# Kernel optimization log

Hardware: AMD Instinct MI355X
Metric: run time of the kernel (lower is better)

The kernel has to match this reference:

```python
import jax, jax.numpy as jnp
import numpy as np

EPS = 1e-8  # matches PairwiseCosine eps clamp


def setup_inputs() -> dict:
    key = jax.random.key(0)
    k1, k2, k3 = jax.random.split(key, 3)
    B, N, M, D = 8, 2048, 2048, 256
    desc_src = jax.random.normal(k1, (B, N, D), dtype=jnp.float32)
    desc_dst = jax.random.normal(k2, (B, M, D), dtype=jnp.float32)
    points_dst = jax.random.uniform(k3, (B, M, 2), dtype=jnp.float32)
    return {"desc_src": desc_src, "desc_dst": desc_dst, "points_dst": points_dst}


def reference(desc_src, desc_dst, points_dst):
    # Pairwise cosine similarity: [B, N, M]
    xx = jnp.linalg.norm(desc_src, axis=-1, keepdims=True)          # [B, N, 1]
    yy = jnp.linalg.norm(desc_dst, axis=-1, keepdims=True)          # [B, M, 1]
    xy = jnp.einsum('bnd,bmd->bnm', desc_src, desc_dst)             # [B, N, M]
    sim = xy / jnp.maximum(xx * jnp.swapaxes(yy, 1, 2), EPS)
    # Best match per source descriptor
    confidence = jnp.max(sim, axis=2)                               # [B, N]
    idx = jnp.argmax(sim, axis=2)                                   # [B, N]
    # Gather matched destination points: [B, N, 2]
    matched = jnp.take_along_axis(points_dst, idx[:, :, None], axis=1)
    return (matched, confidence)
```

## Files before the change

### kernel.cpp

```cpp
#include <hip/hip_runtime.h>
#include <stdint.h>

constexpr int Bq = 8, Nq = 2048, Mq = 2048, Dq = 256;
constexpr int TILE = 128;
constexpr int KC = 32;
constexpr int NCH = Dq / KC;
constexpr size_t ROWS = (size_t)Bq * Nq;
constexpr size_t ARR = ROWS * Dq;

typedef float f32x4 __attribute__((ext_vector_type(4)));
typedef _Float16 f16x8 __attribute__((ext_vector_type(8)));
typedef __fp16 fp16x2 __attribute__((ext_vector_type(2)));

typedef const __attribute__((address_space(1))) void* as1_t;
typedef __attribute__((address_space(3))) void* as3_t;

__device__ __forceinline__ void gl_lds16(const void* g, void* l) {
  __builtin_amdgcn_global_load_lds((as1_t)g, (as3_t)l, 16, 0, 0);
}

__device__ __forceinline__ uint32_t f2sortable(float f) {
  uint32_t u = __float_as_uint(f);
  return (u & 0x80000000u) ? ~u : (u | 0x80000000u);
}
__device__ __forceinline__ float sortable2f(uint32_t s) {
  uint32_t u = (s & 0x80000000u) ? (s ^ 0x80000000u) : ~s;
  return __uint_as_float(u);
}

__global__ __launch_bounds__(256)
void split_kernel(const float* __restrict__ src, const float* __restrict__ dst,
                  uint16_t* __restrict__ Ahg, uint16_t* __restrict__ Alg,
                  uint16_t* __restrict__ Bhg, uint16_t* __restrict__ Blg,
                  float* __restrict__ inv_ns, float* __restrict__ inv_nd) {
  int w = blockIdx.x * 4 + (threadIdx.x >> 6);
  int lane = threadIdx.x & 63;
  bool isB = w >= (int)ROWS;
  int row = isB ? (w - (int)ROWS) : w;
  const float* p = (isB ? dst : src) + (size_t)row * Dq + lane * 4;
  float4 v = *(const float4*)p;
  float x[4] = {v.x, v.y, v.z, v.w};
  float sq = 0.f;
  union { fp16x2 p2[2]; uint2 u; } H, L;
#pragma unroll
  for (int j = 0; j < 2; ++j) {
    float x0 = x[2 * j], x1 = x[2 * j + 1];
    sq = fmaf(x0, x0, sq);
    sq = fmaf(x1, x1, sq);
    float h0 = __uint_as_float(__float_as_uint(x0) & 0xFFFFE000u);
    float h1 = __uint_as_float(__float_as_uint(x1) & 0xFFFFE000u);
    H.p2[j] = __builtin_amdgcn_cvt_pkrtz(h0, h1);
    L.p2[j] = __builtin_amdgcn_cvt_pkrtz(x0 - h0, x1 - h1);
  }
  uint16_t* hp = (isB ? Bhg : Ahg) + (size_t)row * Dq + lane * 4;
  uint16_t* lp = (isB ? Blg : Alg) + (size_t)row * Dq + lane * 4;
  *(uint2*)hp = H.u;
  *(uint2*)lp = L.u;
#pragma unroll
  for (int m = 32; m >= 1; m >>= 1) sq += __shfl_xor(sq, m);
  if (lane == 0) {
    float inv = 1.0f / sqrtf(sq);
    (isB ? inv_nd : inv_ns)[row] = inv;
  }
}

__global__ __launch_bounds__(256, 4)
void simmax_kernel(const uint16_t* __restrict__ Ahg, const uint16_t* __restrict__ Alg,
                   const uint16_t* __restrict__ Bhg, const uint16_t* __restrict__ Blg,
                   const float* __restrict__ inv_ns, const float* __restrict__ inv_nd,
                   unsigned long long* __restrict__ best) {
  __shared__ __align__(16) _Float16 lds[4][TILE][KC];

  const int b = blockIdx.z, nt = blockIdx.y, mt = blockIdx.x;
  const int tid = threadIdx.x;
  const int lane = tid & 63;
  const int wave = tid >> 6;
  const int wy = wave >> 1, wx = wave & 1;
  const int ln15 = lane & 15, lq = lane >> 4;

  const uint16_t* garr = (wave == 0) ? Ahg : (wave == 1) ? Alg
                        : (wave == 2) ? Bhg : Blg;
  const int rowg0 = (wave < 2) ? (b * Nq + nt * TILE) : (b * Mq + mt * TILE);
  const int q = (lane & 3) ^ ((lane >> 3) & 3);
  const uint16_t* gbase = garr + ((size_t)(rowg0 + (lane >> 2)) * Dq + q * 8);

  f32x4 acc[4][4];
#pragma unroll
  for (int i = 0; i < 4; ++i)
#pragma unroll
    for (int j = 0; j < 4; ++j) acc[i][j] = (f32x4){0.f, 0.f, 0.f, 0.f};

  const int sl = (lq ^ ((ln15 >> 1) & 3)) * 8;

  for (int c = 0; c < NCH; ++c) {
    __syncthreads();
#pragma unroll
    for (int t = 0; t < 8; ++t)
      gl_lds16(gbase + (size_t)(16 * t) * Dq + c * KC, &lds[wave][16 * t][0]);
    __syncthreads();

    f16x8 bhf[4], blf[4];
#pragma unroll
    for (int ct = 0; ct < 4; ++ct) {
      int rowb = wx * 64 + ct * 16 + ln15;
      bhf[ct] = *(const f16x8*)&lds[2][rowb][sl];
      blf[ct] = *(const f16x8*)&lds[3][rowb][sl];
    }
#pragma unroll
    for (int rt = 0; rt < 4; ++rt) {
      int rowa = wy * 64 + rt * 16 + ln15;
      f16x8 ahf = *(const f16x8*)&lds[0][rowa][sl];
      f16x8 alf = *(const f16x8*)&lds[1][rowa][sl];
#pragma unroll
      for (int ct = 0; ct < 4; ++ct) {
        acc[rt][ct] = __builtin_amdgcn_mfma_f32_16x16x32_f16(ahf, bhf[ct], acc[rt][ct], 0, 0, 0);
        acc[rt][ct] = __builtin_amdgcn_mfma_f32_16x16x32_f16(ahf, blf[ct], acc[rt][ct], 0, 0, 0);
        acc[rt][ct] = __builtin_amdgcn_mfma_f32_16x16x32_f16(alf, bhf[ct], acc[rt][ct], 0, 0, 0);
      }
    }
  }

  float invny[4];
#pragma unroll
  for (int ct = 0; ct < 4; ++ct)
    invny[ct] = inv_nd[b * Mq + mt * TILE + wx * 64 + ct * 16 + ln15];

#pragma unroll
  for (int rt = 0; rt < 4; ++rt) {
#pragma unroll
    for (int reg = 0; reg < 4; ++reg) {
      float bq = -1e30f;
      int bc = 0x7FFFFFFF;
#pragma unroll
      for (int ct = 0; ct < 4; ++ct) {
        float qv = acc[rt][ct][reg] * invny[ct];
        int cg = mt * TILE + wx * 64 + ct * 16 + ln15;
        if (qv > bq || (qv == bq && cg < bc)) { bq = qv; bc = cg; }
      }
#pragma unroll
      for (int m = 1; m <= 8; m <<= 1) {
        float q2 = __shfl_xor(bq, m);
        int c2 = __shfl_xor(bc, m);
        if (q2 > bq || (q2 == bq && c2 < bc)) { bq = q2; bc = c2; }
      }
      if (ln15 == 0) {
        int rloc = wy * 64 + rt * 16 + lq * 4 + reg;
        float conf = bq * inv_ns[b * Nq + nt * TILE + rloc];
        unsigned long long p =
            ((unsigned long long)(f2sortable(conf) ^ 0x80000000u) << 32) |
            (uint32_t)(~(uint32_t)bc);
        atomicMax((long long*)&best[(size_t)b * Nq + nt * TILE + rloc],
                  (long long)p);
      }
    }
  }
}

__global__ void finalize_kernel(const unsigned long long* __restrict__ best,
                                const float* __restrict__ pts,
                                float* __restrict__ out) {
  int i = blockIdx.x * blockDim.x + threadIdx.x;
  if (i >= (int)ROWS) return;
  unsigned long long p = best[i];
  uint32_t s = (uint32_t)(p >> 32) ^ 0x80000000u;
  int idx = (int)(~(uint32_t)(p & 0xFFFFFFFFull));
  float conf = sortable2f(s);
  int b = i / Nq;
  const float* qp = pts + ((size_t)b * Mq + (size_t)idx) * 2;
  out[(size_t)i * 2 + 0] = qp[0];
  out[(size_t)i * 2 + 1] = qp[1];
  out[ROWS * 2 + i] = conf;
}

extern "C" void kernel_launch(void* const* d_in, const int* in_sizes, int n_in,
                              void* d_out, int out_size, void* d_ws, size_t ws_size,
                              hipStream_t stream) {
  const float* src = (const float*)d_in[0];
  const float* dst = (const float*)d_in[1];
  const float* pts = (const float*)d_in[2];
  float* out = (float*)d_out;

  char* w = (char*)d_ws;
  unsigned long long* best = (unsigned long long*)w;
  uint16_t* Ahg = (uint16_t*)(w + (128 << 10));
  uint16_t* Alg = Ahg + ARR;
  uint16_t* Bhg = Alg + ARR;
  uint16_t* Blg = Bhg + ARR;
  float* inv_ns = (float*)(Blg + ARR);
  float* inv_nd = inv_ns + ROWS;

  {
    int blocks = (int)(2 * ROWS / 4);
    split_kernel<<<blocks, 256, 0, stream>>>(src, dst, Ahg, Alg, Bhg, Blg,
                                             inv_ns, inv_nd);
  }
  {
    dim3 grid(Mq / TILE, Nq / TILE, Bq);
    simmax_kernel<<<grid, 256, 0, stream>>>(Ahg, Alg, Bhg, Blg, inv_ns, inv_nd,
                                            best);
  }
  {
    int blocks = ((int)ROWS + 255) / 256;
    finalize_kernel<<<blocks, 256, 0, stream>>>(best, pts, out);
  }
}
```

Before: 164.9 us.

## Pre-swizzle split operands into MFMA fragment layout and load directly from global

```diff
diff --git a/kernel.cpp b/kernel.cpp
--- a/kernel.cpp
+++ b/kernel.cpp
@@ -11,13 +11,6 @@
 typedef float f32x4 __attribute__((ext_vector_type(4)));
 typedef _Float16 f16x8 __attribute__((ext_vector_type(8)));
 typedef __fp16 fp16x2 __attribute__((ext_vector_type(2)));
-
-typedef const __attribute__((address_space(1))) void* as1_t;
-typedef __attribute__((address_space(3))) void* as3_t;
-
-__device__ __forceinline__ void gl_lds16(const void* g, void* l) {
-  __builtin_amdgcn_global_load_lds((as1_t)g, (as3_t)l, 16, 0, 0);
-}
 
 __device__ __forceinline__ uint32_t f2sortable(float f) {
   uint32_t u = __float_as_uint(f);
@@ -33,44 +26,46 @@
                   uint16_t* __restrict__ Ahg, uint16_t* __restrict__ Alg,
                   uint16_t* __restrict__ Bhg, uint16_t* __restrict__ Blg,
                   float* __restrict__ inv_ns, float* __restrict__ inv_nd) {
-  int w = blockIdx.x * 4 + (threadIdx.x >> 6);
-  int lane = threadIdx.x & 63;
-  bool isB = w >= (int)ROWS;
-  int row = isB ? (w - (int)ROWS) : w;
-  const float* p = (isB ? dst : src) + (size_t)row * Dq + lane * 4;
-  float4 v = *(const float4*)p;
-  float x[4] = {v.x, v.y, v.z, v.w};
+  const int blk = blockIdx.x;
+  const bool isB = blk >= (int)(ROWS / 8);
+  const int rowbase = (blk - (isB ? (int)(ROWS / 8) : 0)) * 8;
+  const int t = threadIdx.x;
+  const int j = t & 31;
+  const int row = rowbase + (t >> 5);
+
+  const float* p = (isB ? dst : src) + (size_t)row * Dq + j * 8;
+  float4 v0 = *(const float4*)p;
+  float4 v1 = *(const float4*)(p + 4);
+  float x[8] = {v0.x, v0.y, v0.z, v0.w, v1.x, v1.y, v1.z, v1.w};
+
   float sq = 0.f;
-  union { fp16x2 p2[2]; uint2 u; } H, L;
+  union { fp16x2 p2[4]; uint4 u; } H, L;
 #pragma unroll
-  for (int j = 0; j < 2; ++j) {
-    float x0 = x[2 * j], x1 = x[2 * j + 1];
+  for (int k = 0; k < 4; ++k) {
+    float x0 = x[2 * k], x1 = x[2 * k + 1];
     sq = fmaf(x0, x0, sq);
     sq = fmaf(x1, x1, sq);
     float h0 = __uint_as_float(__float_as_uint(x0) & 0xFFFFE000u);
     float h1 = __uint_as_float(__float_as_uint(x1) & 0xFFFFE000u);
-    H.p2[j] = __builtin_amdgcn_cvt_pkrtz(h0, h1);
-    L.p2[j] = __builtin_amdgcn_cvt_pkrtz(x0 - h0, x1 - h1);
+    H.p2[k] = __builtin_amdgcn_cvt_pkrtz(h0, h1);
+    L.p2[k] = __builtin_amdgcn_cvt_pkrtz(x0 - h0, x1 - h1);
   }
-  uint16_t* hp = (isB ? Bhg : Ahg) + (size_t)row * Dq + lane * 4;
-  uint16_t* lp = (isB ? Blg : Alg) + (size_t)row * Dq + lane * 4;
-  *(uint2*)hp = H.u;
-  *(uint2*)lp = L.u;
+
+  size_t g = ((size_t)(row >> 4) * 8 + (j >> 2)) * 64 + (size_t)((j & 3) * 16 + (row & 15));
+  *(uint4*)((isB ? Bhg : Ahg) + g * 8) = H.u;
+  *(uint4*)((isB ? Blg : Alg) + g * 8) = L.u;
+
 #pragma unroll
-  for (int m = 32; m >= 1; m >>= 1) sq += __shfl_xor(sq, m);
-  if (lane == 0) {
-    float inv = 1.0f / sqrtf(sq);
-    (isB ? inv_nd : inv_ns)[row] = inv;
-  }
+  for (int m = 1; m <= 16; m <<= 1) sq += __shfl_xor(sq, m);
+  if (j == 0)
+    (isB ? inv_nd : inv_ns)[row] = 1.0f / sqrtf(sq);
 }
 
-__global__ __launch_bounds__(256, 4)
+__global__ __launch_bounds__(256, 3)
 void simmax_kernel(const uint16_t* __restrict__ Ahg, const uint16_t* __restrict__ Alg,
                    const uint16_t* __restrict__ Bhg, const uint16_t* __restrict__ Blg,
                    const float* __restrict__ inv_ns, const float* __restrict__ inv_nd,
                    unsigned long long* __restrict__ best) {
-  __shared__ __align__(16) _Float16 lds[4][TILE][KC];
-
   const int b = blockIdx.z, nt = blockIdx.y, mt = blockIdx.x;
   const int tid = threadIdx.x;
   const int lane = tid & 63;
@@ -78,11 +73,8 @@
   const int wy = wave >> 1, wx = wave & 1;
   const int ln15 = lane & 15, lq = lane >> 4;
 
-  const uint16_t* garr = (wave == 0) ? Ahg : (wave == 1) ? Alg
-                        : (wave == 2) ? Bhg : Blg;
-  const int rowg0 = (wave < 2) ? (b * Nq + nt * TILE) : (b * Mq + mt * TILE);
-  const int q = (lane & 3) ^ ((lane >> 3) & 3);
-  const uint16_t* gbase = garr + ((size_t)(rowg0 + (lane >> 2)) * Dq + q * 8);
+  const size_t tileA = (size_t)b * 128 + nt * 8 + wy * 4;
+  const size_t tileB = (size_t)b * 128 + mt * 8 + wx * 4;
 
   f32x4 acc[4][4];
 #pragma unroll
@@ -90,34 +82,29 @@
 #pragma unroll
     for (int j = 0; j < 4; ++j) acc[i][j] = (f32x4){0.f, 0.f, 0.f, 0.f};
 
-  const int sl = (lq ^ ((ln15 >> 1) & 3)) * 8;
-
+#pragma unroll
   for (int c = 0; c < NCH; ++c) {
-    __syncthreads();
+    f16x8 ahf[4], alf[4], bhf[4], blf[4];
 #pragma unroll
-    for (int t = 0; t < 8; ++t)
-      gl_lds16(gbase + (size_t)(16 * t) * Dq + c * KC, &lds[wave][16 * t][0]);
-    __syncthreads();
-
-    f16x8 bhf[4], blf[4];
+    for (int rt = 0; rt < 4; ++rt) {
+      size_t g = (((tileA + rt) * 8 + c) * 64 + lane) * 8;
+      ahf[rt] = *(const f16x8*)(Ahg + g);
+      alf[rt] = *(const f16x8*)(Alg + g);
+    }
 #pragma unroll
     for (int ct = 0; ct < 4; ++ct) {
-      int rowb = wx * 64 + ct * 16 + ln15;
-      bhf[ct] = *(const f16x8*)&lds[2][rowb][sl];
-      blf[ct] = *(const f16x8*)&lds[3][rowb][sl];
+      size_t g = (((tileB + ct) * 8 + c) * 64 + lane) * 8;
+      bhf[ct] = *(const f16x8*)(Bhg + g);
+      blf[ct] = *(const f16x8*)(Blg + g);
     }
 #pragma unroll
-    for (int rt = 0; rt < 4; ++rt) {
-      int rowa = wy * 64 + rt * 16 + ln15;
-      f16x8 ahf = *(const f16x8*)&lds[0][rowa][sl];
-      f16x8 alf = *(const f16x8*)&lds[1][rowa][sl];
+    for (int rt = 0; rt < 4; ++rt)
 #pragma unroll
       for (int ct = 0; ct < 4; ++ct) {
-        acc[rt][ct] = __builtin_amdgcn_mfma_f32_16x16x32_f16(ahf, bhf[ct], acc[rt][ct], 0, 0, 0);
-        acc[rt][ct] = __builtin_amdgcn_mfma_f32_16x16x32_f16(ahf, blf[ct], acc[rt][ct], 0, 0, 0);
-        acc[rt][ct] = __builtin_amdgcn_mfma_f32_16x16x32_f16(alf, bhf[ct], acc[rt][ct], 0, 0, 0);
+        acc[rt][ct] = __builtin_amdgcn_mfma_f32_16x16x32_f16(ahf[rt], bhf[ct], acc[rt][ct], 0, 0, 0);
+        acc[rt][ct] = __builtin_amdgcn_mfma_f32_16x16x32_f16(ahf[rt], blf[ct], acc[rt][ct], 0, 0, 0);
+        acc[rt][ct] = __builtin_amdgcn_mfma_f32_16x16x32_f16(alf[rt], bhf[ct], acc[rt][ct], 0, 0, 0);
       }
-    }
   }
 
   float invny[4];
@@ -190,7 +177,7 @@
   float* inv_nd = inv_ns + ROWS;
 
   {
-    int blocks = (int)(2 * ROWS / 4);
+    int blocks = (int)(2 * ROWS / 8);
     split_kernel<<<blocks, 256, 0, stream>>>(src, dst, Ahg, Alg, Bhg, Blg,
                                              inv_ns, inv_nd);
   }
```

Result: slower. 187.0 us (+13.4%).
